# Performance work log

Hardware: AMD Instinct MI355X
Metric: run time of the kernel (lower is better)

Reference implementation:

```python
import jax, jax.numpy as jnp
import numpy as np

EMB = 1024
HEADS = 16
FFN = 4096
EPS = 1e-5


def _layernorm(x, g, b):
    mu = jnp.mean(x, axis=-1, keepdims=True)
    var = jnp.mean((x - mu) ** 2, axis=-1, keepdims=True)
    return (x - mu) * jax.lax.rsqrt(var + EPS) * g + b


def setup_inputs() -> dict:
    key = jax.random.key(0)
    ks = jax.random.split(key, 8)
    B, T = 2, 2048
    s_in = 1.0 / np.sqrt(EMB)
    s_ffn = 1.0 / np.sqrt(FFN)
    return {
        "x": jax.random.normal(ks[0], (B, T, EMB), jnp.float32),
        "positions": jnp.arange(B * T, dtype=jnp.int64 if jax.config.jax_enable_x64 else jnp.int32).reshape(B, T),
        "ln1_g": jnp.ones((EMB,), jnp.float32),
        "ln1_b": jnp.zeros((EMB,), jnp.float32),
        "ln2_g": jnp.ones((EMB,), jnp.float32),
        "ln2_b": jnp.zeros((EMB,), jnp.float32),
        "Wq": jax.random.normal(ks[1], (EMB, EMB), jnp.float32) * s_in,
        "bq": jnp.zeros((EMB,), jnp.float32),
        "Wk": jax.random.normal(ks[2], (EMB, EMB), jnp.float32) * s_in,
        "bk": jnp.zeros((EMB,), jnp.float32),
        "Wv": jax.random.normal(ks[3], (EMB, EMB), jnp.float32) * s_in,
        "bv": jnp.zeros((EMB,), jnp.float32),
        "Wo": jax.random.normal(ks[4], (EMB, EMB), jnp.float32) * s_in,
        "bo": jnp.zeros((EMB,), jnp.float32),
        "W1": jax.random.normal(ks[5], (EMB, FFN), jnp.float32) * s_in,
        "b1": jnp.zeros((FFN,), jnp.float32),
        "W2": jax.random.normal(ks[6], (FFN, EMB), jnp.float32) * s_ffn,
        "b2": jnp.zeros((EMB,), jnp.float32),
    }


def reference(x, positions, ln1_g, ln1_b, ln2_g, ln2_b,
              Wq, bq, Wk, bk, Wv, bv, Wo, bo, W1, b1, W2, b2):
    B, T, C = x.shape
    H, D = HEADS, C // HEADS
    # x = ln1(x); then residual branches add onto the normalized x (as in source)
    x = _layernorm(x, ln1_g, ln1_b)
    # --- self attention (rope=None, mask=None, dropout inactive) ---
    q = (x @ Wq + bq).reshape(B, T, H, D).transpose(0, 2, 1, 3)  # [B,H,T,D]
    k = (x @ Wk + bk).reshape(B, T, H, D).transpose(0, 2, 1, 3)
    v = (x @ Wv + bv).reshape(B, T, H, D).transpose(0, 2, 1, 3)
    scale = 1.0 / jnp.sqrt(jnp.asarray(D, x.dtype))
    attn = jnp.einsum("bhtd,bhsd->bhts", q, k) * scale  # [B,H,T,T]
    attn = jax.nn.softmax(attn, axis=-1)
    attn_out = jnp.einsum("bhts,bhsd->bhtd", attn, v)
    attn_out = attn_out.transpose(0, 2, 1, 3).reshape(B, T, C)
    attn_out = attn_out @ Wo + bo
    x = x + attn_out
    # --- FFN with exact (erf) GELU, matching torch nn.GELU default ---
    h = _layernorm(x, ln2_g, ln2_b)
    h = jax.nn.gelu(h @ W1 + b1, approximate=False)
    h = h @ W2 + b2
    return x + h
```

## Files before the change

### kernel.cpp

```cpp
#include <hip/hip_runtime.h>
#include <cstdint>
#include <cstddef>

typedef __bf16 bf16;
typedef __bf16 bf16x8 __attribute__((ext_vector_type(8)));
typedef __bf16 bf16x4 __attribute__((ext_vector_type(4)));
typedef float f32x4 __attribute__((ext_vector_type(4)));

#define TOKENS 4096
#define TSEQ   2048
#define NHEADS 16
#define HDIM   64
#define CDIM   1024

typedef __attribute__((address_space(3))) unsigned int lds_uint;
typedef __attribute__((address_space(1))) const unsigned int g_uint;
__device__ __forceinline__ void glds16(const bf16* g, bf16* l) {
  __builtin_amdgcn_global_load_lds((g_uint*)g, (lds_uint*)l, 16, 0, 0);
}

__device__ __forceinline__ float gelu_f(float v) {
  float g2 = v * (1.5957691216f + 0.0713548163f * v * v);
  return v / (1.0f + __expf(-g2));
}

#define NBUF 17
struct DetectArgs { const void* p[NBUF]; int n[NBUF]; };

__global__ __launch_bounds__(256) void detect_kernel(DetectArgs a, int* __restrict__ flags) {
  __shared__ int s_nz, s_bl;
  if (threadIdx.x == 0) { s_nz = 0; s_bl = 0; }
  __syncthreads();
  int i = blockIdx.x;
  const unsigned int* w = (const unsigned int*)a.p[i];
  int nwords = a.n[i] / 2; if (nwords > 2048) nwords = 2048;
  int nz = 0, bl = 0;
  for (int j = threadIdx.x; j < nwords; j += 256) {
    unsigned int v = w[j];
    if (v != 0u) {
      nz++;
      unsigned int e = (v >> 7) & 0xFFu;
      if (e >= 100u && e <= 140u) bl++;
    }
  }
  atomicAdd(&s_nz, nz);
  atomicAdd(&s_bl, bl);
  __syncthreads();
  if (threadIdx.x == 0) flags[i] = (2 * s_bl >= s_nz) ? 1 : 0;
}

__device__ __forceinline__ float ld_any(const void* p, size_t idx, bool isb) {
  return isb ? (float)((const bf16*)p)[idx] : ((const float*)p)[idx];
}

__device__ __forceinline__ void ln_stats(float s, float s2, int tid, float& mu, float& rstd) {
#pragma unroll
  for (int off = 32; off; off >>= 1) {
    s  += __shfl_down(s, off);
    s2 += __shfl_down(s2, off);
  }
  __shared__ float red[8];
  int w = tid >> 6;
  if ((tid & 63) == 0) { red[w] = s; red[4 + w] = s2; }
  __syncthreads();
  if (tid == 0) {
    red[0] = red[0] + red[1] + red[2] + red[3];
    red[4] = red[4] + red[5] + red[6] + red[7];
  }
  __syncthreads();
  mu = red[0] * (1.0f / CDIM);
  float var = fmaxf(red[4] * (1.0f / CDIM) - mu * mu, 0.f);
  rstd = rsqrtf(var + 1e-5f);
}

__global__ __launch_bounds__(256) void ln_f32(const float* __restrict__ x,
                                              const bf16* __restrict__ g,
                                              const bf16* __restrict__ b,
                                              bf16* __restrict__ y) {
  int row = blockIdx.x, tid = threadIdx.x;
  float v[4]; float s = 0.f, s2 = 0.f;
#pragma unroll
  for (int i = 0; i < 4; i++) {
    float f = x[(size_t)row * CDIM + tid * 4 + i];
    v[i] = f; s += f; s2 += f * f;
  }
  float mu, rstd;
  ln_stats(s, s2, tid, mu, rstd);
  bf16* yr = y + (size_t)row * CDIM;
#pragma unroll
  for (int i = 0; i < 4; i++) {
    int c = tid * 4 + i;
    yr[c] = (bf16)((v[i] - mu) * rstd * (float)g[c] + (float)b[c]);
  }
}

struct MegaArgs {
  const void* w_in[6]; bf16* w_out[6]; int wK[6], wN[6], wflag[6];
  const void* vp[10]; bf16* vd[10]; int vn[10], vfi[10];
  const void* x; const void* graw; const void* braw; bf16* y;
};

__global__ __launch_bounds__(256) void mega_pre(MegaArgs a, const int* __restrict__ flags) {
  int bid = blockIdx.x;
  int tx = threadIdx.x, ty = threadIdx.y;
  int tid = tx + ty * 64;
  if (bid < 3072) {
    __shared__ bf16 tile[64][65];
    int mi, start;
    if (bid < 1024)      { mi = bid >> 8; start = mi << 8; }
    else if (bid < 2048) { mi = 4; start = 1024; }
    else                 { mi = 5; start = 2048; }
    int tb = bid - start;
    int nT = a.wN[mi] >> 6;
    int kb = (tb / nT) * 64, nb = (tb % nT) * 64;
    int K = a.wK[mi], N = a.wN[mi];
    bool isb = flags[a.wflag[mi]] != 0;
    const void* in = a.w_in[mi]; bf16* out = a.w_out[mi];
    for (int i = ty; i < 64; i += 4)
      tile[i][tx] = (bf16)ld_any(in, (size_t)(kb + i) * N + nb + tx, isb);
    __syncthreads();
    for (int i = ty; i < 64; i += 4)
      out[(size_t)(nb + i) * K + kb + tx] = tile[tx][i];
  } else if (bid == 3072) {
    for (int i = 0; i < 10; i++) {
      bool isb = flags[a.vfi[i]] != 0;
      const void* in = a.vp[i]; bf16* out = a.vd[i]; int n = a.vn[i];
      for (int j = tid; j < n; j += 256)
        out[j] = (bf16)ld_any(in, j, isb);
    }
  } else {
    int row = bid - 3073;
    bool isb  = flags[0] != 0;
    bool gisb = flags[1] != 0;
    bool bisb = flags[2] != 0;
    float v[4]; float s = 0.f, s2 = 0.f;
#pragma unroll
    for (int i = 0; i < 4; i++) {
      float f = ld_any(a.x, (size_t)row * CDIM + tid * 4 + i, isb);
      v[i] = f; s += f; s2 += f * f;
    }
    float mu, rstd;
    ln_stats(s, s2, tid, mu, rstd);
    bf16* yr = a.y + (size_t)row * CDIM;
#pragma unroll
    for (int i = 0; i < 4; i++) {
      int c = tid * 4 + i;
      float gv = ld_any(a.graw, c, gisb);
      float bv = ld_any(a.braw, c, bisb);
      yr[c] = (bf16)((v[i] - mu) * rstd * gv + bv);
    }
  }
}

template <int BM, int BN>
__device__ __forceinline__ void gemm_core(const bf16* __restrict__ A,
                                          const bf16* __restrict__ Bt,
                                          int K, int m0, int n0,
                                          bf16* As, bf16* Bs,
                                          f32x4 (&acc)[BM / 32][BN / 32]) {
  constexpr int SI = BM / 32, SJ = BN / 32;
  int t = threadIdx.x;
  int wave = t >> 6, lane = t & 63, quad = lane >> 4, l16 = lane & 15;
  int wm = (wave & 1) * (BM / 2), wn = (wave >> 1) * (BN / 2);
  int srow = t >> 2, sc = t & 3;
  int swz = (srow >> 1) & 3;
  const bf16* ga[BM / 64];
  const bf16* gb[BN / 64];
#pragma unroll
  for (int h = 0; h < BM / 64; h++)
    ga[h] = A + (size_t)(m0 + h * 64 + srow) * K + (sc ^ swz) * 8;
#pragma unroll
  for (int h = 0; h < BN / 64; h++)
    gb[h] = Bt + (size_t)(n0 + h * 64 + srow) * K + (sc ^ swz) * 8;

  for (int k0 = 0; k0 < K; k0 += 64) {
#pragma unroll
    for (int q = 0; q < 2; q++) {
#pragma unroll
      for (int h = 0; h < BM / 64; h++)
        glds16(ga[h] + k0 + q * 32, As + q * (BM * 32) + h * 2048 + srow * 32 + sc * 8);
#pragma unroll
      for (int h = 0; h < BN / 64; h++)
        glds16(gb[h] + k0 + q * 32, Bs + q * (BN * 32) + h * 2048 + srow * 32 + sc * 8);
    }
    __syncthreads();
#pragma unroll
    for (int q = 0; q < 2; q++) {
      bf16x8 af[SI], bfr[SJ];
#pragma unroll
      for (int i = 0; i < SI; i++) {
        int m = wm + i * 16 + l16;
        af[i] = *(const bf16x8*)&As[q * (BM * 32) + m * 32 + ((quad ^ ((m >> 1) & 3)) * 8)];
      }
#pragma unroll
      for (int j = 0; j < SJ; j++) {
        int n = wn + j * 16 + l16;
        bfr[j] = *(const bf16x8*)&Bs[q * (BN * 32) + n * 32 + ((quad ^ ((n >> 1) & 3)) * 8)];
      }
#pragma unroll
      for (int i = 0; i < SI; i++)
#pragma unroll
        for (int j = 0; j < SJ; j++)
          acc[i][j] = __builtin_amdgcn_mfma_f32_16x16x32_bf16(af[i], bfr[j], acc[i][j], 0, 0, 0);
    }
    __syncthreads();
  }
}

#define EPI_NONE 0
#define EPI_RES  1
#define EPI_GELU 2

template <int BM, int BN, int EPI, typename OutT, typename ResT>
__global__ __launch_bounds__(256) void gemm128(const bf16* __restrict__ A,
                                               const bf16* __restrict__ Bt,
                                               const bf16* __restrict__ bias,
                                               const ResT* __restrict__ res,
                                               OutT* __restrict__ C,
                                               int N, int K) {
  __shared__ alignas(16) bf16 As[2 * BM * 32];
  __shared__ alignas(16) bf16 Bs[2 * BN * 32];
  int m0 = blockIdx.y * BM, n0 = blockIdx.x * BN;
  f32x4 acc[BM / 32][BN / 32] = {};
  gemm_core<BM, BN>(A, Bt, K, m0, n0, As, Bs, acc);

  int t = threadIdx.x, wave = t >> 6, lane = t & 63, quad = lane >> 4, l16 = lane & 15;
  int wm = (wave & 1) * (BM / 2), wn = (wave >> 1) * (BN / 2);
#pragma unroll
  for (int i = 0; i < BM / 32; i++)
#pragma unroll
    for (int j = 0; j < BN / 32; j++) {
      int n = n0 + wn + j * 16 + l16;
      float bv = (float)bias[n];
#pragma unroll
      for (int r = 0; r < 4; r++) {
        int m = m0 + wm + i * 16 + quad * 4 + r;
        float v = acc[i][j][r] + bv;
        if (EPI == EPI_GELU)      v = gelu_f(v);
        else if (EPI == EPI_RES)  v += (float)res[(size_t)m * N + n];
        C[(size_t)m * N + n] = (OutT)v;
      }
    }
}

__global__ __launch_bounds__(256) void gemm_qkv(const bf16* __restrict__ A,
                                                const bf16* __restrict__ Bt,
                                                const bf16* __restrict__ bias,
                                                bf16* __restrict__ QK,
                                                bf16* __restrict__ Vt) {
  __shared__ alignas(16) bf16 As[2 * 128 * 32];
  __shared__ alignas(16) bf16 Bs[2 * 128 * 32];
  int m0 = blockIdx.y * 128, n0 = blockIdx.x * 128;
  f32x4 acc[4][4] = {};
  gemm_core<128, 128>(A, Bt, 1024, m0, n0, As, Bs, acc);

  int t = threadIdx.x, wave = t >> 6, lane = t & 63, quad = lane >> 4, l16 = lane & 15;
  int wm = (wave & 1) * 64, wn = (wave >> 1) * 64;
#pragma unroll
  for (int i = 0; i < 4; i++)
#pragma unroll
    for (int j = 0; j < 4; j++) {
      int n = n0 + wn + j * 16 + l16;
      float bv = (float)bias[n];
      int mb = m0 + wm + i * 16 + quad * 4;
      if (n < 1024) {
#pragma unroll
        for (int r = 0; r < 4; r++)
          QK[(size_t)(mb + r) * 2048 + n] = (bf16)((acc[i][j][r] + bv) * 0.125f);
      } else if (n < 2048) {
#pragma unroll
        for (int r = 0; r < 4; r++)
          QK[(size_t)(mb + r) * 2048 + n] = (bf16)(acc[i][j][r] + bv);
      } else {
        bf16x4 pk;
#pragma unroll
        for (int r = 0; r < 4; r++) pk[r] = (bf16)(acc[i][j][r] + bv);
        *(bf16x4*)&Vt[(size_t)(n - 2048) * TOKENS + mb] = pk;
      }
    }
}

__global__ __launch_bounds__(512) void attn_kernel(const bf16* __restrict__ QK,
                                                   const bf16* __restrict__ Vt,
                                                   bf16* __restrict__ O) {
  __shared__ alignas(16) bf16 Ks[2][4096];
  __shared__ alignas(16) bf16 Vs[2][4096];
  __shared__ alignas(16) bf16 Ps[8][16 * 72];
  int b = blockIdx.z, h = blockIdx.y, q0 = blockIdx.x * 128;
  int t = threadIdx.x, wave = t >> 6, lane = t & 63, quad = lane >> 4, l16 = lane & 15;

  const bf16* Qg = QK;
  const bf16* Kg = QK + 1024;
  const size_t bT = (size_t)b * TSEQ;
  const int h64 = h * 64;

  int srow = wave * 8 + (lane >> 3);
  int schunk = (lane & 7) ^ (srow & 7);

  bf16x8 aq0, aq1;
  {
    size_t qrow = bT + q0 + wave * 16 + l16;
    aq0 = *(const bf16x8*)&Qg[qrow * 2048 + h64 + quad * 8];
    aq1 = *(const bf16x8*)&Qg[qrow * 2048 + h64 + 32 + quad * 8];
  }

  f32x4 accO[4] = {};
  f32x4 accL = {};

  auto stage = [&](int tile, int buf) {
    glds16(&Kg[(bT + tile * 64 + srow) * 2048 + h64 + schunk * 8],
           &Ks[buf][wave * 512 + lane * 8]);
    glds16(&Vt[(size_t)(h64 + srow) * TOKENS + bT + tile * 64 + schunk * 8],
           &Vs[buf][wave * 512 + lane * 8]);
  };

  const bf16 one = (bf16)1.0f;
  const bf16x8 onesv = {one, one, one, one, one, one, one, one};
  int sw = l16 & 7;
  bf16* Pw = &Ps[wave][0];

  stage(0, 0);
  __syncthreads();

  for (int it = 0; it < TSEQ / 64; it++) {
    int cur = it & 1;
    if (it + 1 < TSEQ / 64) stage(it + 1, cur ^ 1);

    const bf16* KsC = &Ks[cur][0];
    const bf16* VsC = &Vs[cur][0];

    f32x4 S[4];
#pragma unroll
    for (int c = 0; c < 4; c++) {
      int row = c * 16 + l16;
      bf16x8 kb0 = *(const bf16x8*)&KsC[row * 64 + ((quad ^ sw) * 8)];
      bf16x8 kb1 = *(const bf16x8*)&KsC[row * 64 + (((quad + 4) ^ sw) * 8)];
      f32x4 s = {};
      s = __builtin_amdgcn_mfma_f32_16x16x32_bf16(aq0, kb0, s, 0, 0, 0);
      s = __builtin_amdgcn_mfma_f32_16x16x32_bf16(aq1, kb1, s, 0, 0, 0);
      S[c] = s;
    }

#pragma unroll
    for (int c = 0; c < 4; c++)
#pragma unroll
      for (int r = 0; r < 4; r++)
        Pw[(quad * 4 + r) * 72 + c * 16 + l16] = (bf16)__expf(fminf(S[c][r], 60.f));

    bf16x8 pa0 = *(const bf16x8*)&Pw[l16 * 72 + quad * 8];
    bf16x8 pa1 = *(const bf16x8*)&Pw[l16 * 72 + 32 + quad * 8];
#pragma unroll
    for (int ds = 0; ds < 4; ds++) {
      int row = ds * 16 + l16;
      bf16x8 vb0 = *(const bf16x8*)&VsC[row * 64 + ((quad ^ sw) * 8)];
      bf16x8 vb1 = *(const bf16x8*)&VsC[row * 64 + (((quad + 4) ^ sw) * 8)];
      accO[ds] = __builtin_amdgcn_mfma_f32_16x16x32_bf16(pa0, vb0, accO[ds], 0, 0, 0);
      accO[ds] = __builtin_amdgcn_mfma_f32_16x16x32_bf16(pa1, vb1, accO[ds], 0, 0, 0);
    }
    accL = __builtin_amdgcn_mfma_f32_16x16x32_bf16(pa0, onesv, accL, 0, 0, 0);
    accL = __builtin_amdgcn_mfma_f32_16x16x32_bf16(pa1, onesv, accL, 0, 0, 0);

    __syncthreads();
  }

#pragma unroll
  for (int ds = 0; ds < 4; ds++)
#pragma unroll
    for (int r = 0; r < 4; r++) {
      float v = accO[ds][r] / fmaxf(accL[r], 1e-30f);
      O[(bT + q0 + wave * 16 + quad * 4 + r) * CDIM + h64 + ds * 16 + l16] = (bf16)v;
    }
}

extern "C" void kernel_launch(void* const* d_in, const int* in_sizes, int n_in,
                              void* d_out, int out_size, void* d_ws, size_t ws_size,
                              hipStream_t stream) {
  char* ws = (char*)d_ws;
  const size_t MB = 1024 * 1024;
  const size_t KB = 1024;

  int* flags = (int*)ws;
  bf16* vec_c = (bf16*)(ws + 4 * KB);
  bf16* ln1g_c = vec_c + 0 * 8192;
  bf16* ln1b_c = vec_c + 1 * 8192;
  bf16* ln2g_c = vec_c + 2 * 8192;
  bf16* ln2b_c = vec_c + 3 * 8192;
  bf16* bqkv_c = vec_c + 4 * 8192;
  bf16* bo_c   = vec_c + 6 * 8192;
  bf16* b1_c   = vec_c + 7 * 8192;
  bf16* b2_c   = vec_c + 8 * 8192;

  bf16*  WqkvT  = (bf16*)(ws + 1 * MB);
  bf16*  WoT    = (bf16*)(ws + 7 * MB);
  bf16*  W1T    = (bf16*)(ws + 9 * MB);
  bf16*  W2T    = (bf16*)(ws + 17 * MB);
  bf16*  xn     = (bf16*)(ws + 25 * MB);
  bf16*  QKbuf  = (bf16*)(ws + 33 * MB);
  bf16*  Vtbuf  = (bf16*)(ws + 49 * MB);
  bf16*  ab     = (bf16*)(ws + 57 * MB);
  float* xmid32 = (float*)(ws + 65 * MB);
  bf16*  h2     = (bf16*)(ws + 81 * MB);
  bf16*  f1     = (bf16*)(ws + 33 * MB);

  const int din_idx[NBUF] = {0, 2, 3, 4, 5, 6, 7, 8, 9, 10, 11, 12, 13, 14, 15, 16, 17};
  DetectArgs da;
  for (int i = 0; i < NBUF; i++) { da.p[i] = d_in[din_idx[i]]; da.n[i] = in_sizes[din_idx[i]]; }
  detect_kernel<<<NBUF, 256, 0, stream>>>(da, flags);

  MegaArgs ma;
  {
    const void* wi[6] = {d_in[6], d_in[8], d_in[10], d_in[12], d_in[14], d_in[16]};
    bf16* wo[6] = {WqkvT, WqkvT + 1024 * 1024, WqkvT + 2 * 1024 * 1024, WoT, W1T, W2T};
    const int wK[6] = {1024, 1024, 1024, 1024, 1024, 4096};
    const int wN[6] = {1024, 1024, 1024, 1024, 4096, 1024};
    const int wf[6] = {5, 7, 9, 11, 13, 15};
    for (int i = 0; i < 6; i++) {
      ma.w_in[i] = wi[i]; ma.w_out[i] = wo[i];
      ma.wK[i] = wK[i]; ma.wN[i] = wN[i]; ma.wflag[i] = wf[i];
    }
    const int vf[10] = {1, 2, 3, 4, 6, 8, 10, 12, 14, 16};
    bf16* vd[10] = {ln1g_c, ln1b_c, ln2g_c, ln2b_c,
                    bqkv_c, bqkv_c + 1024, bqkv_c + 2048, bo_c, b1_c, b2_c};
    for (int i = 0; i < 10; i++) {
      int di = din_idx[vf[i]];
      ma.vp[i] = d_in[di]; ma.vd[i] = vd[i]; ma.vn[i] = in_sizes[di]; ma.vfi[i] = vf[i];
    }
    ma.x = d_in[0]; ma.graw = d_in[2]; ma.braw = d_in[3]; ma.y = xn;
  }
  mega_pre<<<3072 + 1 + TOKENS, dim3(64, 4), 0, stream>>>(ma, flags);

  gemm_qkv<<<dim3(24, 32), 256, 0, stream>>>(xn, WqkvT, bqkv_c, QKbuf, Vtbuf);

  attn_kernel<<<dim3(TSEQ / 128, NHEADS, 2), 512, 0, stream>>>(QKbuf, Vtbuf, ab);

  gemm128<64, 128, EPI_RES, float, bf16><<<dim3(8, 64), 256, 0, stream>>>(
      ab, WoT, bo_c, xn, xmid32, 1024, 1024);

  ln_f32<<<TOKENS, 256, 0, stream>>>(xmid32, ln2g_c, ln2b_c, h2);

  gemm128<128, 128, EPI_GELU, bf16, bf16><<<dim3(32, 32), 256, 0, stream>>>(
      h2, W1T, b1_c, (const bf16*)nullptr, f1, 4096, 1024);

  gemm128<64, 128, EPI_RES, float, float><<<dim3(8, 64), 256, 0, stream>>>(
      f1, W2T, b2_c, xmid32, (float*)d_out, 1024, 4096);
}
```

Before: 394.4 us.

## Use 256x256-tile 8-wave pipelined GEMM with XCD swizzle for QKV and FFN1

Adds a new GEMM core with 256x256 output tiles, 8 waves, a K-step of 64, and double-buffered LDS filled by direct global-to-LDS loads. Loads are staged across four compute phases with barriers, setprio, and a swizzled LDS layout to avoid bank conflicts. An XCD-aware block remap groups neighbouring tiles on the same die. The QKV projection and the GELU FFN1 GEMM move to this core to raise data reuse per block and overlap memory with MFMA. The cost is far fewer blocks (192 and 256), which may underfill the 256 CUs, plus 128KB of LDS per block and high register pressure.

```diff
diff --git a/kernel.cpp b/kernel.cpp
--- a/kernel.cpp
+++ b/kernel.cpp
@@ -243,21 +243,148 @@
     }
 }
 
-__global__ __launch_bounds__(256) void gemm_qkv(const bf16* __restrict__ A,
-                                                const bf16* __restrict__ Bt,
-                                                const bf16* __restrict__ bias,
-                                                bf16* __restrict__ QK,
-                                                bf16* __restrict__ Vt) {
-  __shared__ alignas(16) bf16 As[2 * 128 * 32];
-  __shared__ alignas(16) bf16 Bs[2 * 128 * 32];
-  int m0 = blockIdx.y * 128, n0 = blockIdx.x * 128;
-  f32x4 acc[4][4] = {};
-  gemm_core<128, 128>(A, Bt, 1024, m0, n0, As, Bs, acc);
+__device__ __forceinline__ void gemm256_core(const bf16* __restrict__ A,
+                                             const bf16* __restrict__ Bt,
+                                             int K, int m0, int n0,
+                                             bf16* sm, f32x4 (&acc)[8][4]) {
+  const int NT = K >> 6;
+  const int t = threadIdx.x;
+  const int lane = t & 63, quad = lane >> 4, l16 = lane & 15;
+  const int wave = t >> 6;
+  const int wm = (wave & 1) * 128, wn = (wave >> 1) * 64;
+  const int srow = t >> 2, sc = t & 3;
+  const int swz = (srow >> 1) & 3;
+  const int rA = (srow & 63) + ((srow >> 6) << 7);
+  const bf16* gA = A + (size_t)(m0 + rA) * K + ((sc ^ swz) << 3);
+  const bf16* gB = Bt + (size_t)(n0 + srow) * K + ((sc ^ swz) << 3);
+  const int ldsA = rA * 32 + sc * 8;
+  const int ldsB = srow * 32 + sc * 8;
+
+  auto stA = [&](int tile, int u) {
+    if (tile >= NT) return;
+    const bf16* g = gA + (size_t)(u << 6) * K + (tile << 6);
+    bf16* l = sm + ((tile & 1) << 15) + ldsA + (u << 11);
+    glds16(g, l);
+    glds16(g + 32, l + 8192);
+  };
+  auto stB = [&](int tile, int h) {
+    if (tile >= NT) return;
+    const bf16* g = gB + (size_t)(h << 7) * K + (tile << 6);
+    bf16* l = sm + ((tile & 1) << 15) + 16384 + ldsB + (h << 12);
+    glds16(g, l);
+    glds16(g + 32, l + 8192);
+  };
+
+  stB(0, 0); stB(0, 1); stA(0, 0); stA(0, 1);
+  stB(1, 0); stB(1, 1); stA(1, 0);
+  asm volatile("s_waitcnt vmcnt(6)" ::: "memory");
+  __builtin_amdgcn_s_barrier();
+  asm volatile("" ::: "memory");
+
+  bf16x8 bfr[2][4];
+
+#define LDB256(buf)                                                        \
+  _Pragma("unroll") for (int q = 0; q < 2; q++)                            \
+  _Pragma("unroll") for (int j = 0; j < 4; j++) {                          \
+    int nl = wn + j * 16 + l16;                                            \
+    bfr[q][j] = *(const bf16x8*)&sm[((buf) << 15) + 16384 + q * 8192 +     \
+                                    nl * 32 + ((quad ^ ((nl >> 1) & 3)) << 3)]; \
+  }
+
+#define PHASE256(buf, P, STAGE, EXTRAWAIT)                                 \
+  {                                                                        \
+    bf16x8 af[2][2];                                                       \
+    _Pragma("unroll") for (int q = 0; q < 2; q++)                          \
+    _Pragma("unroll") for (int i2 = 0; i2 < 2; i2++) {                     \
+      int ml = wm + (P) * 32 + i2 * 16 + l16;                              \
+      af[q][i2] = *(const bf16x8*)&sm[((buf) << 15) + q * 8192 + ml * 32 + \
+                                      ((quad ^ ((ml >> 1) & 3)) << 3)];    \
+    }                                                                      \
+    if ((P) == 0) { LDB256(buf); }                                         \
+    STAGE;                                                                 \
+    asm volatile("" ::: "memory");                                         \
+    __builtin_amdgcn_s_barrier();                                          \
+    asm volatile("s_waitcnt lgkmcnt(0)" ::: "memory");                     \
+    __builtin_amdgcn_s_setprio(1);                                         \
+    _Pragma("unroll") for (int q = 0; q < 2; q++)                          \
+    _Pragma("unroll") for (int i2 = 0; i2 < 2; i2++)                       \
+    _Pragma("unroll") for (int j = 0; j < 4; j++)                          \
+      acc[(P) * 2 + i2][j] = __builtin_amdgcn_mfma_f32_16x16x32_bf16(      \
+          af[q][i2], bfr[q][j], acc[(P) * 2 + i2][j], 0, 0, 0);            \
+    __builtin_amdgcn_s_setprio(0);                                         \
+    asm volatile("" ::: "memory");                                         \
+    EXTRAWAIT;                                                             \
+    __builtin_amdgcn_s_barrier();                                          \
+    asm volatile("" ::: "memory");                                         \
+  }
+
+  for (int t0 = 0; t0 < NT; t0 += 2) {
+    const int t1 = t0 + 1;
+    PHASE256(0, 0, stA(t1, 1), (void)0);
+    PHASE256(0, 1, stB(t0 + 2, 0), (void)0);
+    PHASE256(0, 2, stB(t0 + 2, 1), (void)0);
+    PHASE256(0, 3, stA(t0 + 2, 0),
+             asm volatile("s_waitcnt vmcnt(6)" ::: "memory"));
+    PHASE256(1, 0, stA(t0 + 2, 1), (void)0);
+    PHASE256(1, 1, stB(t1 + 2, 0), (void)0);
+    PHASE256(1, 2, stB(t1 + 2, 1), (void)0);
+    PHASE256(1, 3, stA(t1 + 2, 0),
+             asm volatile("s_waitcnt vmcnt(6)" ::: "memory"));
+  }
+#undef PHASE256
+#undef LDB256
+}
+
+__device__ __forceinline__ void xcd_swizzle(int& bx, int& by) {
+  int gx = gridDim.x;
+  int nwg = gx * gridDim.y;
+  int bid = blockIdx.x + blockIdx.y * gx;
+  int wg = (bid & 7) * (nwg >> 3) + (bid >> 3);
+  bx = wg % gx; by = wg / gx;
+}
+
+__global__ __launch_bounds__(512, 2) void gemm256_gelu(const bf16* __restrict__ A,
+                                                       const bf16* __restrict__ Bt,
+                                                       const bf16* __restrict__ bias,
+                                                       bf16* __restrict__ C,
+                                                       int N, int K) {
+  __shared__ alignas(16) bf16 sm[65536];
+  int bx, by; xcd_swizzle(bx, by);
+  int m0 = by * 256, n0 = bx * 256;
+  f32x4 acc[8][4] = {};
+  gemm256_core(A, Bt, K, m0, n0, sm, acc);
 
   int t = threadIdx.x, wave = t >> 6, lane = t & 63, quad = lane >> 4, l16 = lane & 15;
-  int wm = (wave & 1) * 64, wn = (wave >> 1) * 64;
-#pragma unroll
-  for (int i = 0; i < 4; i++)
+  int wm = (wave & 1) * 128, wn = (wave >> 1) * 64;
+#pragma unroll
+  for (int i = 0; i < 8; i++)
+#pragma unroll
+    for (int j = 0; j < 4; j++) {
+      int n = n0 + wn + j * 16 + l16;
+      float bv = (float)bias[n];
+#pragma unroll
+      for (int r = 0; r < 4; r++) {
+        int m = m0 + wm + i * 16 + quad * 4 + r;
+        C[(size_t)m * N + n] = (bf16)gelu_f(acc[i][j][r] + bv);
+      }
+    }
+}
+
+__global__ __launch_bounds__(512, 2) void gemm256_qkv(const bf16* __restrict__ A,
+                                                      const bf16* __restrict__ Bt,
+                                                      const bf16* __restrict__ bias,
+                                                      bf16* __restrict__ QK,
+                                                      bf16* __restrict__ Vt) {
+  __shared__ alignas(16) bf16 sm[65536];
+  int bx, by; xcd_swizzle(bx, by);
+  int m0 = by * 256, n0 = bx * 256;
+  f32x4 acc[8][4] = {};
+  gemm256_core(A, Bt, 1024, m0, n0, sm, acc);
+
+  int t = threadIdx.x, wave = t >> 6, lane = t & 63, quad = lane >> 4, l16 = lane & 15;
+  int wm = (wave & 1) * 128, wn = (wave >> 1) * 64;
+#pragma unroll
+  for (int i = 0; i < 8; i++)
 #pragma unroll
     for (int j = 0; j < 4; j++) {
       int n = n0 + wn + j * 16 + l16;
@@ -429,7 +556,7 @@
   }
   mega_pre<<<3072 + 1 + TOKENS, dim3(64, 4), 0, stream>>>(ma, flags);
 
-  gemm_qkv<<<dim3(24, 32), 256, 0, stream>>>(xn, WqkvT, bqkv_c, QKbuf, Vtbuf);
+  gemm256_qkv<<<dim3(12, 16), 512, 0, stream>>>(xn, WqkvT, bqkv_c, QKbuf, Vtbuf);
 
   attn_kernel<<<dim3(TSEQ / 128, NHEADS, 2), 512, 0, stream>>>(QKbuf, Vtbuf, ab);
 
@@ -438,8 +565,7 @@
 
   ln_f32<<<TOKENS, 256, 0, stream>>>(xmid32, ln2g_c, ln2b_c, h2);
 
-  gemm128<128, 128, EPI_GELU, bf16, bf16><<<dim3(32, 32), 256, 0, stream>>>(
-      h2, W1T, b1_c, (const bf16*)nullptr, f1, 4096, 1024);
+  gemm256_gelu<<<dim3(16, 16), 512, 0, stream>>>(h2, W1T, b1_c, f1, 4096, 1024);
 
   gemm128<64, 128, EPI_RES, float, float><<<dim3(8, 64), 256, 0, stream>>>(
       f1, W2T, b2_c, xmid32, (float*)d_out, 1024, 4096);
```

Result: faster. 384.2 us (-2.6%).
